# Performance work log

Hardware: AMD Instinct MI355X
Metric: run time of the kernel (lower is better)

Reference implementation:

```python
import jax, jax.numpy as jnp
import numpy as np

N = 50000      # nodes
E = 1600000    # edges
D = 128        # input_dim
H = 128        # hidden_dim
C = 10         # n_class
G = 512        # number of graphs (max(idx)+1)
LRELU_ALPHA = 0.05
BN_EPS = 1e-5


def setup_inputs() -> dict:
    key = jax.random.key(0)
    ks = jax.random.split(key, 10)
    x_in = jax.random.normal(ks[0], (N, D), dtype=jnp.float32)
    edge_index = jax.random.randint(ks[1], (2, E), 0, N, dtype=jnp.int32)
    idx = jnp.sort(jax.random.randint(ks[2], (N,), 0, G, dtype=jnp.int32))

    def lin(k, shape, fan_in):
        return jax.random.normal(k, shape, dtype=jnp.float32) / np.sqrt(fan_in).astype(np.float32)

    fc_w = lin(ks[3], (H, D), D)        # GATLayer.fc weight
    a1 = lin(ks[4], (H,), 2 * H)        # a weight, src half
    a2 = lin(ks[5], (H,), 2 * H)        # a weight, dst half
    fc1_w = lin(ks[6], (H, H), H)
    fc1_b = jnp.zeros((H,), jnp.float32)
    fc2_w = lin(ks[7], (C, H), H)
    fc2_b = jnp.zeros((C,), jnp.float32)
    gamma = jnp.ones((H,), jnp.float32)  # BatchNorm weight
    beta = jnp.zeros((H,), jnp.float32)  # BatchNorm bias
    return {"x_in": x_in, "edge_index": edge_index, "idx": idx,
            "fc_w": fc_w, "a1": a1, "a2": a2,
            "fc1_w": fc1_w, "fc1_b": fc1_b, "fc2_w": fc2_w, "fc2_b": fc2_b,
            "gamma": gamma, "beta": beta}


def reference(x_in, edge_index, idx, fc_w, a1, a2, fc1_w, fc1_b, fc2_w, fc2_b, gamma, beta):
    # input standardization (torch.std is unbiased -> ddof=1)
    x = (x_in - jnp.mean(x_in)) / jnp.std(x_in, ddof=1)

    # ---- GAT layer ----
    z = x @ fc_w.T                              # [N, H]
    src, dst = edge_index[0], edge_index[1]
    # a([z_src ; z_dst]) == z_src@a1 + z_dst@a2  (avoids materializing [E, 2H])
    s1 = z @ a1                                  # [N]
    s2 = z @ a2                                  # [N]
    e = s1[src] + s2[dst]                        # [E]
    e = jnp.where(e >= 0, e, LRELU_ALPHA * e)    # LeakyReLU(0.05)
    h = jnp.exp(e)
    h_sum = jax.ops.segment_sum(h, src, num_segments=N)   # edge-softmax denom per src row
    alpha = h / h_sum[src]                       # [E]
    # sparse.mm(adj_att, z): out[src] += alpha * z[dst]
    out = jax.ops.segment_sum(alpha[:, None] * z[dst], src, num_segments=N)  # [N, H]

    x = jax.nn.relu(out)
    # dropout: identity (eval / deterministic reference)

    # sum pooling per graph
    pooled = jax.ops.segment_sum(x, idx, num_segments=G)   # [G, H]

    # BatchNorm1d (training-mode batch statistics, biased var)
    mu = jnp.mean(pooled, axis=0)
    var = jnp.var(pooled, axis=0)
    xb = (pooled - mu) / jnp.sqrt(var + BN_EPS) * gamma + beta

    x = jax.nn.relu(xb @ fc1_w.T + fc1_b)
    logits = x @ fc2_w.T + fc2_b
    return jax.nn.log_softmax(logits, axis=1)
```

## Files before the change

kernel.cpp:

```cpp
#include <hip/hip_runtime.h>

#define NN 50000
#define NE 1600000
#define DD 128
#define HH 128
#define CC 10
#define GG 512
#define LRELU_A 0.05f
#define BN_EPS 1e-5f

#define TT 256
#define EPT (NE / TT)
#define NBR 782
#define NBP 784
#define NPB 64
#define KNODE 8
#define STB 1024

typedef unsigned int u32;
typedef unsigned short u16;
typedef unsigned char u8;
typedef __attribute__((ext_vector_type(8))) short bf16x8;
typedef __attribute__((ext_vector_type(4))) float f32x4;

__device__ __forceinline__ u16 f2bf(float f) {
    u32 u = __float_as_uint(f);
    u32 r = u + 0x7FFFu + ((u >> 16) & 1u);
    return (u16)(r >> 16);
}
__device__ __forceinline__ float bf2f(u32 lo16) {
    return __uint_as_float(lo16 << 16);
}

__global__ __launch_bounds__(256) void k_front(const int* __restrict__ src,
                                               const float* __restrict__ x,
                                               u16* __restrict__ cnt_b,
                                               u8* __restrict__ rank_e,
                                               float* __restrict__ pooled,
                                               double* __restrict__ pst) {
    __shared__ u32 h[NBP];
    __shared__ double ls[4], lss[4];
    int bid = blockIdx.x, tid = threadIdx.x;
    if (bid < TT) {
        for (int i = tid; i < NBP; i += 256) h[i] = 0;
        pooled[bid * 256 + tid] = 0.f;
        __syncthreads();
        int e0 = bid * EPT;
        for (int i = tid; i < EPT; i += 256) {
            int b = src[e0 + i] >> 6;
            u32 old = atomicAdd(&h[b], 1u);
            rank_e[e0 + i] = (u8)old;
        }
        __syncthreads();
        for (int i = tid; i < NBP; i += 256) cnt_b[bid * NBP + i] = (u16)h[i];
    } else {
        int sb = bid - TT;
        const int M4 = NN * DD / 4;
        double s = 0.0, ss = 0.0;
        for (int i = sb * 256 + tid; i < M4; i += STB * 256) {
            float4 v = reinterpret_cast<const float4*>(x)[i];
            s  += (double)v.x + (double)v.y + (double)v.z + (double)v.w;
            ss += (double)v.x * v.x + (double)v.y * v.y + (double)v.z * v.z +
                  (double)v.w * v.w;
        }
        for (int d = 32; d; d >>= 1) { s += __shfl_down(s, d); ss += __shfl_down(ss, d); }
        int lane = tid & 63, w = tid >> 6;
        if (lane == 0) { ls[w] = s; lss[w] = ss; }
        __syncthreads();
        if (tid == 0) {
            pst[2 * sb]     = ls[0] + ls[1] + ls[2] + ls[3];
            pst[2 * sb + 1] = lss[0] + lss[1] + lss[2] + lss[3];
        }
    }
}

__global__ __launch_bounds__(256) void k_mid(const u16* __restrict__ cnt_b,
                                             const double* __restrict__ pst,
                                             const float* __restrict__ fc_w,
                                             u16* __restrict__ rel_b,
                                             int* __restrict__ base_b,
                                             float* __restrict__ wsum,
                                             float* __restrict__ musig,
                                             u16* __restrict__ wbf) {
    int t = threadIdx.x;
    int bid = blockIdx.x;
    if (bid == 0) {
        __shared__ int sm[256];
        __shared__ int runs;
        if (t == 0) runs = 0;
        __syncthreads();
        for (int chunk = 0; chunk < 4; ++chunk) {
            int b = chunk * 256 + t;
            int tot = 0;
            if (b < NBP)
                for (int tt = 0; tt < TT; ++tt) tot += cnt_b[tt * NBP + b];
            sm[t] = tot;
            __syncthreads();
            for (int d = 1; d < 256; d <<= 1) {
                int x = 0;
                if (t >= d) x = sm[t - d];
                __syncthreads();
                if (t >= d) sm[t] += x;
                __syncthreads();
            }
            if (b < NBP) base_b[b] = runs + sm[t] - tot;
            __syncthreads();
            if (t == 255) runs += sm[255];
            __syncthreads();
        }
        if (t == 0) base_b[NBP] = runs;
    } else if (bid <= 4) {
        int b = (bid - 1) * 196 + t;
        if (t < 196) {
            int run = 0;
            for (int tt = 0; tt < TT; ++tt) {
                int c = cnt_b[tt * NBP + b];
                rel_b[tt * NBP + b] = (u16)run;
                run += c;
            }
        }
    } else {
        __shared__ double rs[256], rss[256];
        double s  = pst[2 * t] + pst[2 * (t + 256)] + pst[2 * (t + 512)] + pst[2 * (t + 768)];
        double ss = pst[2 * t + 1] + pst[2 * (t + 256) + 1] +
                    pst[2 * (t + 512) + 1] + pst[2 * (t + 768) + 1];
        rs[t] = s; rss[t] = ss;
        __syncthreads();
        for (int d = 128; d; d >>= 1) {
            if (t < d) { rs[t] += rs[t + d]; rss[t] += rss[t + d]; }
            __syncthreads();
        }
        if (t == 0) {
            double M = (double)NN * DD;
            double mean = rs[0] / M;
            double var  = (rss[0] - rs[0] * rs[0] / M) / (M - 1.0);
            musig[0] = (float)mean;
            musig[1] = (float)(1.0 / sqrt(var));
        }
        for (int i = t; i < DD * HH; i += 256) wbf[i] = f2bf(fc_w[i]);
        if (t < 128) {
            float acc = 0.f;
            for (int k = 0; k < DD; ++k)
                acc += bf2f(f2bf(fc_w[t * DD + k]));
            wsum[t] = acc;
        }
    }
}

#define XP 136
__global__ __launch_bounds__(256) void k_big(const int* __restrict__ src,
                                             const int* __restrict__ dst,
                                             const u16* __restrict__ rel_b,
                                             const u8* __restrict__ rank_e,
                                             const int* __restrict__ base_b,
                                             u32* __restrict__ ebuf,
                                             const float* __restrict__ x,
                                             const u16* __restrict__ wbf,
                                             const float* __restrict__ wsum,
                                             const float* __restrict__ musig,
                                             const float* __restrict__ a1,
                                             const float* __restrict__ a2,
                                             u32* __restrict__ zbf,
                                             float* __restrict__ s1,
                                             float* __restrict__ s2) {
    __shared__ u16 xls[64 * XP];
    int bid = blockIdx.x, tid = threadIdx.x;

    if (bid < TT) {
        int e0 = bid * EPT;
        for (int i = tid; i < EPT; i += 256) {
            int s = src[e0 + i];
            int b = s >> 6;
            int pos = base_b[b] + (int)rel_b[bid * NBP + b] + (int)rank_e[e0 + i];
            ebuf[pos] = ((u32)dst[e0 + i] << 6) | (u32)(s & 63);
        }
        return;
    }

    int row0 = (bid - TT) * 64;
    for (int i = tid; i < 64 * 32; i += 256) {
        int r = i >> 5, m = i & 31;
        int gr = row0 + r;
        float4 v = (gr < NN) ? reinterpret_cast<const float4*>(x)[gr * 32 + m]
                             : make_float4(0.f, 0.f, 0.f, 0.f);
        u32 p0 = ((u32)f2bf(v.y) << 16) | f2bf(v.x);
        u32 p1 = ((u32)f2bf(v.w) << 16) | f2bf(v.z);
        *reinterpret_cast<uint2*>(&xls[r * XP + m * 4]) = make_uint2(p0, p1);
    }
    __syncthreads();

    int w = tid >> 6, l = tid & 63;
    int lrow = l & 15, lk = l >> 4;

    bf16x8 af[4];
    #pragma unroll
    for (int kc = 0; kc < 4; ++kc)
        af[kc] = *reinterpret_cast<const bf16x8*>(
            &xls[(w * 16 + lrow) * XP + kc * 32 + lk * 8]);

    f32x4 acc[8];
    #pragma unroll
    for (int nt = 0; nt < 8; ++nt) acc[nt] = (f32x4){0.f, 0.f, 0.f, 0.f};

    #pragma unroll
    for (int nt = 0; nt < 8; ++nt) {
        #pragma unroll
        for (int kc = 0; kc < 4; ++kc) {
            bf16x8 bfr = *reinterpret_cast<const bf16x8*>(
                &wbf[(nt * 16 + lrow) * DD + kc * 32 + lk * 8]);
            acc[nt] = __builtin_amdgcn_mfma_f32_16x16x32_bf16(af[kc], bfr,
                                                              acc[nt], 0, 0, 0);
        }
    }
    __syncthreads();

    float mu = musig[0], isig = musig[1];
    #pragma unroll
    for (int nt = 0; nt < 8; ++nt) {
        int col = nt * 16 + lrow;
        float wsc = wsum[col];
        #pragma unroll
        for (int r = 0; r < 4; ++r) {
            int lr = w * 16 + lk * 4 + r;
            float z = (acc[nt][r] - mu * wsc) * isig;
            xls[lr * XP + col] = f2bf(z);
        }
    }
    __syncthreads();

    {
        int r = tid >> 2, q = tid & 3;
        int gr = row0 + r;
        const uint4* lz = reinterpret_cast<const uint4*>(&xls[r * XP + q * 32]);
        uint4 c0 = lz[0], c1 = lz[1], c2 = lz[2], c3 = lz[3];
        if (gr < NN) {
            uint4* zb = reinterpret_cast<uint4*>(zbf) + gr * 16 + q * 4;
            zb[0] = c0; zb[1] = c1; zb[2] = c2; zb[3] = c3;
        }
        u32 wd[16] = {c0.x, c0.y, c0.z, c0.w, c1.x, c1.y, c1.z, c1.w,
                      c2.x, c2.y, c2.z, c2.w, c3.x, c3.y, c3.z, c3.w};
        const float4* A14 = reinterpret_cast<const float4*>(a1 + q * 32);
        const float4* A24 = reinterpret_cast<const float4*>(a2 + q * 32);
        float p1 = 0.f, p2 = 0.f;
        #pragma unroll
        for (int j = 0; j < 8; ++j) {
            float4 va1 = A14[j], va2 = A24[j];
            u32 wlo = wd[2 * j], whi = wd[2 * j + 1];
            float z0 = bf2f(wlo & 0xFFFFu), z1 = bf2f(wlo >> 16);
            float z2 = bf2f(whi & 0xFFFFu), z3 = bf2f(whi >> 16);
            p1 += z0 * va1.x + z1 * va1.y + z2 * va1.z + z3 * va1.w;
            p2 += z0 * va2.x + z1 * va2.y + z2 * va2.z + z3 * va2.w;
        }
        p1 += __shfl_down(p1, 2, 4); p1 += __shfl_down(p1, 1, 4);
        p2 += __shfl_down(p2, 2, 4); p2 += __shfl_down(p2, 1, 4);
        if (q == 0 && gr < NN) { s1[gr] = p1; s2[gr] = p2; }
    }
}

__global__ __launch_bounds__(256) void k_bcsr(const u32* __restrict__ ebuf,
                                              const int* __restrict__ base_b,
                                              const float* __restrict__ s1,
                                              const float* __restrict__ s2,
                                              int* __restrict__ off,
                                              u32* __restrict__ dst_s) {
    __shared__ u32 hist[NPB];
    __shared__ u32 cur[NPB];
    __shared__ int sm[NPB];
    int b = blockIdx.x, tid = threadIdx.x;
    int ebase = base_b[b], eend = base_b[b + 1];
    int m = eend - ebase;
    if (tid < NPB) hist[tid] = 0;
    __syncthreads();
    for (int i = tid; i < m; i += 256)
        atomicAdd(&hist[ebuf[ebase + i] & 63u], 1u);
    __syncthreads();
    if (tid < NPB) sm[tid] = (int)hist[tid];
    __syncthreads();
    for (int d = 1; d < NPB; d <<= 1) {
        int x = 0;
        if (tid < NPB && tid >= d) x = sm[tid - d];
        __syncthreads();
        if (tid < NPB && tid >= d) sm[tid] += x;
        __syncthreads();
    }
    if (tid < NPB) {
        int v = (int)hist[tid];
        int st = sm[tid] - v;
        cur[tid] = (u32)st;
        int n = b * NPB + tid;
        if (n < NN) off[n] = ebase + st;
    }
    if (b == NBR - 1 && tid == 0) off[NN] = NE;
    __syncthreads();
    for (int i = tid; i < m; i += 256) {
        u32 e = ebuf[ebase + i];
        int ls = (int)(e & 63u);
        int dn = (int)(e >> 6);
        int p = (int)atomicAdd(&cur[ls], 1u);
        float ev = s1[b * NPB + ls] + s2[dn];
        ev = (ev >= 0.f) ? ev : LRELU_A * ev;
        float h = __expf(ev);
        dst_s[ebase + p] = ((u32)dn << 16) | (u32)f2bf(h);
    }
}

__global__ __launch_bounds__(256) void k_aggregate(const u32* __restrict__ zbf,
                                                   const int* __restrict__ off,
                                                   const u32* __restrict__ dst_s,
                                                   const int* __restrict__ idx,
                                                   float* __restrict__ pooled) {
    int wave = (blockIdx.x * 256 + threadIdx.x) >> 6;
    int lane = threadIdx.x & 63;
    int n0 = wave * KNODE;
    if (n0 >= NN) return;
    int n1 = n0 + KNODE;
    if (n1 > NN) n1 = NN;

    float pool0 = 0.f, pool1 = 0.f;
    int curg = idx[n0];

    for (int node = n0; node < n1; ++node) {
        int g = idx[node];
        if (g != curg) {
            atomicAdd(&pooled[curg * HH + lane * 2], pool0);
            atomicAdd(&pooled[curg * HH + lane * 2 + 1], pool1);
            pool0 = 0.f; pool1 = 0.f;
            curg = g;
        }
        int j0 = off[node], j1 = off[node + 1];
        float acc0 = 0.f, acc1 = 0.f, hsl = 0.f;

        for (int b = j0; b < j1; b += 64) {
            int cnt = j1 - b;
            if (cnt > 64) cnt = 64;
            int jj = b + ((lane < cnt) ? lane : 0);
            int ul = (int)dst_s[jj];
            if (lane < cnt) hsl += __uint_as_float((u32)ul << 16);
            int k = 0;
            for (; k + 8 <= cnt; k += 8) {
                int eu[8]; u32 uu[8];
                #pragma unroll
                for (int q = 0; q < 8; ++q) eu[q] = __shfl(ul, k + q);
                #pragma unroll
                for (int q = 0; q < 8; ++q)
                    uu[q] = zbf[(((u32)eu[q] >> 16) << 6) | lane];
                #pragma unroll
                for (int q = 0; q < 8; ++q) {
                    float hq = __uint_as_float((u32)eu[q] << 16);
                    acc0 += hq * __uint_as_float(uu[q] << 16);
                    acc1 += hq * __uint_as_float(uu[q] & 0xFFFF0000u);
                }
            }
            for (; k + 4 <= cnt; k += 4) {
                int eu[4]; u32 uu[4];
                #pragma unroll
                for (int q = 0; q < 4; ++q) eu[q] = __shfl(ul, k + q);
                #pragma unroll
                for (int q = 0; q < 4; ++q)
                    uu[q] = zbf[(((u32)eu[q] >> 16) << 6) | lane];
                #pragma unroll
                for (int q = 0; q < 4; ++q) {
                    float hq = __uint_as_float((u32)eu[q] << 16);
                    acc0 += hq * __uint_as_float(uu[q] << 16);
                    acc1 += hq * __uint_as_float(uu[q] & 0xFFFF0000u);
                }
            }
            for (; k < cnt; ++k) {
                int e = __shfl(ul, k);
                float hk = __uint_as_float((u32)e << 16);
                u32 u = zbf[(((u32)e >> 16) << 6) | lane];
                acc0 += hk * __uint_as_float(u << 16);
                acc1 += hk * __uint_as_float(u & 0xFFFF0000u);
            }
        }
        float hs = hsl;
        #pragma unroll
        for (int d = 32; d; d >>= 1) hs += __shfl_xor(hs, d);
        float inv = (hs > 0.f) ? 1.f / hs : 0.f;
        pool0 += fmaxf(acc0 * inv, 0.f);
        pool1 += fmaxf(acc1 * inv, 0.f);
    }
    atomicAdd(&pooled[curg * HH + lane * 2], pool0);
    atomicAdd(&pooled[curg * HH + lane * 2 + 1], pool1);
}

__global__ __launch_bounds__(128) void k_head(const float* __restrict__ pooled,
                                              const float* __restrict__ gamma,
                                              const float* __restrict__ beta,
                                              const float* __restrict__ fc1w,
                                              const float* __restrict__ fc1b,
                                              const float* __restrict__ fc2w,
                                              const float* __restrict__ fc2b,
                                              float* __restrict__ out) {
    __shared__ __align__(16) float xb[128];
    __shared__ __align__(16) float h1[128];
    __shared__ float lg[16];
    int g = blockIdx.x;
    int t = threadIdx.x;
    float s = 0.f, ss = 0.f;
    #pragma unroll 8
    for (int q = 0; q < GG; ++q) {
        float v = pooled[q * HH + t];
        s += v;
        ss += v * v;
    }
    float mean = s / GG;
    float var  = ss / GG - mean * mean;
    float sc = gamma[t] * rsqrtf(var + BN_EPS);
    xb[t] = pooled[g * HH + t] * sc + (beta[t] - mean * sc);
    __syncthreads();
    float acc = 0.f;
    const float4* wr = reinterpret_cast<const float4*>(&fc1w[t * HH]);
    #pragma unroll 8
    for (int k = 0; k < 32; ++k) {
        float4 w4 = wr[k];
        float4 xv = *reinterpret_cast<const float4*>(&xb[k * 4]);
        acc += w4.x * xv.x + w4.y * xv.y + w4.z * xv.z + w4.w * xv.w;
    }
    acc += fc1b[t];
    h1[t] = (acc > 0.f) ? acc : 0.f;
    __syncthreads();
    if (t < CC) {
        float a = 0.f;
        const float4* w2 = reinterpret_cast<const float4*>(&fc2w[t * HH]);
        #pragma unroll 8
        for (int k = 0; k < 32; ++k) {
            float4 w4 = w2[k];
            float4 hv = *reinterpret_cast<const float4*>(&h1[k * 4]);
            a += w4.x * hv.x + w4.y * hv.y + w4.z * hv.z + w4.w * hv.w;
        }
        lg[t] = a + fc2b[t];
    }
    __syncthreads();
    if (t == 0) {
        float mx = lg[0];
        for (int c = 1; c < CC; ++c) mx = fmaxf(mx, lg[c]);
        float se = 0.f;
        for (int c = 0; c < CC; ++c) se += __expf(lg[c] - mx);
        float lse = mx + logf(se);
        for (int c = 0; c < CC; ++c) out[g * CC + c] = lg[c] - lse;
    }
}

extern "C" void kernel_launch(void* const* d_in, const int* in_sizes, int n_in,
                              void* d_out, int out_size, void* d_ws, size_t ws_size,
                              hipStream_t stream) {
    const float* x_in  = (const float*)d_in[0];
    const int*   eidx  = (const int*)d_in[1];
    const int*   src   = eidx;
    const int*   dst   = eidx + NE;
    const int*   idx   = (const int*)d_in[2];
    const float* fc_w  = (const float*)d_in[3];
    const float* a1    = (const float*)d_in[4];
    const float* a2    = (const float*)d_in[5];
    const float* fc1w  = (const float*)d_in[6];
    const float* fc1b  = (const float*)d_in[7];
    const float* fc2w  = (const float*)d_in[8];
    const float* fc2b  = (const float*)d_in[9];
    const float* gamma = (const float*)d_in[10];
    const float* beta  = (const float*)d_in[11];
    float* out = (float*)d_out;

    char* p = (char*)d_ws;
    auto alloc = [&](size_t bytes) {
        char* r = p;
        p += (bytes + 255) & ~(size_t)255;
        return r;
    };
    double* pst    = (double*)alloc((size_t)STB * 2 * sizeof(double));
    float*  wsum   = (float*)alloc(HH * sizeof(float));
    float*  musig  = (float*)alloc(4 * sizeof(float));
    u16*    wbf    = (u16*)alloc((size_t)DD * HH * sizeof(u16));
    u16*    cnt_b  = (u16*)alloc((size_t)TT * NBP * sizeof(u16));
    u16*    rel_b  = (u16*)alloc((size_t)TT * NBP * sizeof(u16));
    u8*     rank_e = (u8*)alloc((size_t)NE * sizeof(u8));
    int*    base_b = (int*)alloc((NBP + 1) * sizeof(int));
    u32*    ebuf   = (u32*)alloc((size_t)NE * sizeof(u32));
    int*    off    = (int*)alloc((NN + 1) * sizeof(int));
    u32*    dst_s  = (u32*)alloc((size_t)NE * sizeof(u32));
    u32*    zbf    = (u32*)alloc((size_t)NN * (HH / 2) * sizeof(u32));
    float*  s1     = (float*)alloc(NN * sizeof(float));
    float*  s2     = (float*)alloc(NN * sizeof(float));
    float*  pooled = (float*)alloc((size_t)GG * HH * sizeof(float));

    k_front<<<TT + STB, 256, 0, stream>>>(src, x_in, cnt_b, rank_e, pooled, pst);
    k_mid<<<6, 256, 0, stream>>>(cnt_b, pst, fc_w, rel_b, base_b, wsum, musig, wbf);
    int gemm_blocks = (NN + 63) / 64;
    k_big<<<TT + gemm_blocks, 256, 0, stream>>>(src, dst, rel_b, rank_e, base_b,
                                                ebuf, x_in, wbf, wsum, musig,
                                                a1, a2, zbf, s1, s2);
    k_bcsr<<<NBR, 256, 0, stream>>>(ebuf, base_b, s1, s2, off, dst_s);
    int nwaves = (NN + KNODE - 1) / KNODE;
    int nblocks = (nwaves + 3) / 4;
    k_aggregate<<<nblocks, 256, 0, stream>>>(zbf, off, dst_s, idx, pooled);
    k_head<<<GG, 128, 0, stream>>>(pooled, gamma, beta, fc1w, fc1b, fc2w, fc2b, out);
}
```

Baseline: 180.9 us.

## Stage edges locally per tile in front kernel and gather runs in bucket-CSR kernel

Each edge-tile block in the front kernel keeps src and rank in registers, prefix-sums its per-bucket counts and writes edges into a tile-local bucket-sorted staging buffer. This replaces the rank_e array, the serial rel_b prefix pass in k_mid and the global scatter in k_big. k_bcsr then prefix-sums the per-tile counts for its bucket and copies each tile's contiguous run into LDS before building CSR, which removes a scattered global write pass. In exchange the front kernel does extra scan work, and the LDS gather uses serial per-thread loops over uneven runs. It also assumes each bucket holds at most EMAX edges.

```diff
diff --git a/kernel.cpp b/kernel.cpp
--- a/kernel.cpp
+++ b/kernel.cpp
@@ -14,6 +14,7 @@
 #define NBR 782
 #define NBP 784
 #define NPB 64
+#define EMAX 2560
 #define KNODE 8
 #define STB 1024
 
@@ -33,39 +34,76 @@
 }
 
 __global__ __launch_bounds__(256) void k_front(const int* __restrict__ src,
+                                               const int* __restrict__ dst,
                                                const float* __restrict__ x,
                                                u16* __restrict__ cnt_b,
-                                               u8* __restrict__ rank_e,
+                                               u16* __restrict__ tpg,
+                                               u32* __restrict__ stage,
                                                float* __restrict__ pooled,
                                                double* __restrict__ pst) {
     __shared__ u32 h[NBP];
+    __shared__ int tpl[NBP];
+    __shared__ int sm2[256];
+    __shared__ int carry;
     __shared__ double ls[4], lss[4];
     int bid = blockIdx.x, tid = threadIdx.x;
     if (bid < TT) {
         for (int i = tid; i < NBP; i += 256) h[i] = 0;
         pooled[bid * 256 + tid] = 0.f;
+        if (tid == 0) carry = 0;
         __syncthreads();
         int e0 = bid * EPT;
-        for (int i = tid; i < EPT; i += 256) {
-            int b = src[e0 + i] >> 6;
-            u32 old = atomicAdd(&h[b], 1u);
-            rank_e[e0 + i] = (u8)old;
+        int s[25]; int rk[25];
+        #pragma unroll
+        for (int i = 0; i < 25; ++i) {
+            int e = i * 256 + tid;
+            if (e < EPT) {
+                s[i] = src[e0 + e];
+                rk[i] = (int)atomicAdd(&h[s[i] >> 6], 1u);
+            } else s[i] = -1;
         }
         __syncthreads();
         for (int i = tid; i < NBP; i += 256) cnt_b[bid * NBP + i] = (u16)h[i];
+        for (int c = 0; c < 4; ++c) {
+            int b = c * 256 + tid;
+            int v = (b < NBP) ? (int)h[b] : 0;
+            sm2[tid] = v;
+            __syncthreads();
+            for (int d = 1; d < 256; d <<= 1) {
+                int xv = 0;
+                if (tid >= d) xv = sm2[tid - d];
+                __syncthreads();
+                if (tid >= d) sm2[tid] += xv;
+                __syncthreads();
+            }
+            if (b < NBP) tpl[b] = carry + sm2[tid] - v;
+            __syncthreads();
+            if (tid == 255) carry += sm2[255];
+            __syncthreads();
+        }
+        for (int i = tid; i < NBP; i += 256) tpg[bid * NBP + i] = (u16)tpl[i];
+        #pragma unroll
+        for (int i = 0; i < 25; ++i) {
+            int e = i * 256 + tid;
+            if (e < EPT) {
+                int b = s[i] >> 6;
+                int pos = tpl[b] + rk[i];
+                stage[e0 + pos] = ((u32)dst[e0 + e] << 6) | (u32)(s[i] & 63);
+            }
+        }
     } else {
         int sb = bid - TT;
         const int M4 = NN * DD / 4;
-        double s = 0.0, ss = 0.0;
+        double sd = 0.0, ssd = 0.0;
         for (int i = sb * 256 + tid; i < M4; i += STB * 256) {
             float4 v = reinterpret_cast<const float4*>(x)[i];
-            s  += (double)v.x + (double)v.y + (double)v.z + (double)v.w;
-            ss += (double)v.x * v.x + (double)v.y * v.y + (double)v.z * v.z +
-                  (double)v.w * v.w;
-        }
-        for (int d = 32; d; d >>= 1) { s += __shfl_down(s, d); ss += __shfl_down(ss, d); }
+            sd  += (double)v.x + (double)v.y + (double)v.z + (double)v.w;
+            ssd += (double)v.x * v.x + (double)v.y * v.y + (double)v.z * v.z +
+                   (double)v.w * v.w;
+        }
+        for (int d = 32; d; d >>= 1) { sd += __shfl_down(sd, d); ssd += __shfl_down(ssd, d); }
         int lane = tid & 63, w = tid >> 6;
-        if (lane == 0) { ls[w] = s; lss[w] = ss; }
+        if (lane == 0) { ls[w] = sd; lss[w] = ssd; }
         __syncthreads();
         if (tid == 0) {
             pst[2 * sb]     = ls[0] + ls[1] + ls[2] + ls[3];
@@ -77,14 +115,12 @@
 __global__ __launch_bounds__(256) void k_mid(const u16* __restrict__ cnt_b,
                                              const double* __restrict__ pst,
                                              const float* __restrict__ fc_w,
-                                             u16* __restrict__ rel_b,
                                              int* __restrict__ base_b,
                                              float* __restrict__ wsum,
                                              float* __restrict__ musig,
                                              u16* __restrict__ wbf) {
     int t = threadIdx.x;
-    int bid = blockIdx.x;
-    if (bid == 0) {
+    if (blockIdx.x == 0) {
         __shared__ int sm[256];
         __shared__ int runs;
         if (t == 0) runs = 0;
@@ -109,16 +145,6 @@
             __syncthreads();
         }
         if (t == 0) base_b[NBP] = runs;
-    } else if (bid <= 4) {
-        int b = (bid - 1) * 196 + t;
-        if (t < 196) {
-            int run = 0;
-            for (int tt = 0; tt < TT; ++tt) {
-                int c = cnt_b[tt * NBP + b];
-                rel_b[tt * NBP + b] = (u16)run;
-                run += c;
-            }
-        }
     } else {
         __shared__ double rs[256], rss[256];
         double s  = pst[2 * t] + pst[2 * (t + 256)] + pst[2 * (t + 512)] + pst[2 * (t + 768)];
@@ -148,13 +174,7 @@
 }
 
 #define XP 136
-__global__ __launch_bounds__(256) void k_big(const int* __restrict__ src,
-                                             const int* __restrict__ dst,
-                                             const u16* __restrict__ rel_b,
-                                             const u8* __restrict__ rank_e,
-                                             const int* __restrict__ base_b,
-                                             u32* __restrict__ ebuf,
-                                             const float* __restrict__ x,
+__global__ __launch_bounds__(256) void k_big(const float* __restrict__ x,
                                              const u16* __restrict__ wbf,
                                              const float* __restrict__ wsum,
                                              const float* __restrict__ musig,
@@ -166,18 +186,7 @@
     __shared__ u16 xls[64 * XP];
     int bid = blockIdx.x, tid = threadIdx.x;
 
-    if (bid < TT) {
-        int e0 = bid * EPT;
-        for (int i = tid; i < EPT; i += 256) {
-            int s = src[e0 + i];
-            int b = s >> 6;
-            int pos = base_b[b] + (int)rel_b[bid * NBP + b] + (int)rank_e[e0 + i];
-            ebuf[pos] = ((u32)dst[e0 + i] << 6) | (u32)(s & 63);
-        }
-        return;
-    }
-
-    int row0 = (bid - TT) * 64;
+    int row0 = bid * 64;
     for (int i = tid; i < 64 * 32; i += 256) {
         int r = i >> 5, m = i & 31;
         int gr = row0 + r;
@@ -257,22 +266,41 @@
     }
 }
 
-__global__ __launch_bounds__(256) void k_bcsr(const u32* __restrict__ ebuf,
+__global__ __launch_bounds__(256) void k_bcsr(const u32* __restrict__ stage,
+                                              const u16* __restrict__ cnt_b,
+                                              const u16* __restrict__ tpg,
                                               const int* __restrict__ base_b,
                                               const float* __restrict__ s1,
                                               const float* __restrict__ s2,
                                               int* __restrict__ off,
                                               u32* __restrict__ dst_s) {
+    __shared__ u32 eloc[EMAX];
     __shared__ u32 hist[NPB];
     __shared__ u32 cur[NPB];
-    __shared__ int sm[NPB];
+    __shared__ int sm[256];
     int b = blockIdx.x, tid = threadIdx.x;
-    int ebase = base_b[b], eend = base_b[b + 1];
-    int m = eend - ebase;
+    int ebase = base_b[b];
+    int m = base_b[b + 1] - ebase;
+
+    int c_t = (int)cnt_b[tid * NBP + b];
+    int tp0 = (int)tpg[tid * NBP + b];
+    sm[tid] = c_t;
+    __syncthreads();
+    for (int d = 1; d < 256; d <<= 1) {
+        int x = 0;
+        if (tid >= d) x = sm[tid - d];
+        __syncthreads();
+        if (tid >= d) sm[tid] += x;
+        __syncthreads();
+    }
+    int rel = sm[tid] - c_t;
+    const u32* srun = stage + tid * EPT + tp0;
+    for (int r = 0; r < c_t; ++r) eloc[rel + r] = srun[r];
     if (tid < NPB) hist[tid] = 0;
     __syncthreads();
+
     for (int i = tid; i < m; i += 256)
-        atomicAdd(&hist[ebuf[ebase + i] & 63u], 1u);
+        atomicAdd(&hist[eloc[i] & 63u], 1u);
     __syncthreads();
     if (tid < NPB) sm[tid] = (int)hist[tid];
     __syncthreads();
@@ -293,7 +321,7 @@
     if (b == NBR - 1 && tid == 0) off[NN] = NE;
     __syncthreads();
     for (int i = tid; i < m; i += 256) {
-        u32 e = ebuf[ebase + i];
+        u32 e = eloc[i];
         int ls = (int)(e & 63u);
         int dn = (int)(e >> 6);
         int p = (int)atomicAdd(&cur[ls], 1u);
@@ -472,10 +500,9 @@
     float*  musig  = (float*)alloc(4 * sizeof(float));
     u16*    wbf    = (u16*)alloc((size_t)DD * HH * sizeof(u16));
     u16*    cnt_b  = (u16*)alloc((size_t)TT * NBP * sizeof(u16));
-    u16*    rel_b  = (u16*)alloc((size_t)TT * NBP * sizeof(u16));
-    u8*     rank_e = (u8*)alloc((size_t)NE * sizeof(u8));
+    u16*    tpg    = (u16*)alloc((size_t)TT * NBP * sizeof(u16));
     int*    base_b = (int*)alloc((NBP + 1) * sizeof(int));
-    u32*    ebuf   = (u32*)alloc((size_t)NE * sizeof(u32));
+    u32*    stage  = (u32*)alloc((size_t)NE * sizeof(u32));
     int*    off    = (int*)alloc((NN + 1) * sizeof(int));
     u32*    dst_s  = (u32*)alloc((size_t)NE * sizeof(u32));
     u32*    zbf    = (u32*)alloc((size_t)NN * (HH / 2) * sizeof(u32));
@@ -483,13 +510,13 @@
     float*  s2     = (float*)alloc(NN * sizeof(float));
     float*  pooled = (float*)alloc((size_t)GG * HH * sizeof(float));
 
-    k_front<<<TT + STB, 256, 0, stream>>>(src, x_in, cnt_b, rank_e, pooled, pst);
-    k_mid<<<6, 256, 0, stream>>>(cnt_b, pst, fc_w, rel_b, base_b, wsum, musig, wbf);
+    k_front<<<TT + STB, 256, 0, stream>>>(src, dst, x_in, cnt_b, tpg, stage,
+                                          pooled, pst);
+    k_mid<<<2, 256, 0, stream>>>(cnt_b, pst, fc_w, base_b, wsum, musig, wbf);
     int gemm_blocks = (NN + 63) / 64;
-    k_big<<<TT + gemm_blocks, 256, 0, stream>>>(src, dst, rel_b, rank_e, base_b,
-                                                ebuf, x_in, wbf, wsum, musig,
-                                                a1, a2, zbf, s1, s2);
-    k_bcsr<<<NBR, 256, 0, stream>>>(ebuf, base_b, s1, s2, off, dst_s);
+    k_big<<<gemm_blocks, 256, 0, stream>>>(x_in, wbf, wsum, musig,
+                                           a1, a2, zbf, s1, s2);
+    k_bcsr<<<NBR, 256, 0, stream>>>(stage, cnt_b, tpg, base_b, s1, s2, off, dst_s);
     int nwaves = (NN + KNODE - 1) / KNODE;
     int nblocks = (nwaves + 3) / 4;
     k_aggregate<<<nblocks, 256, 0, stream>>>(zbf, off, dst_s, idx, pooled);
```

Result: slower. 187.4 us (+3.6%).
